# Kernel optimization log

Hardware: AMD Instinct MI355X
Metric: run time of the kernel (lower is better)

Reference implementation:

```python
import jax, jax.numpy as jnp
import numpy as np

N, E = 25000, 400000
NIN, NOUT, HID = 32, 32, 128


def setup_inputs() -> dict:
    key = jax.random.key(0)
    ks = jax.random.split(key, 8)
    s = lambda d: 1.0 / np.sqrt(d)
    return {
        "x": jax.random.normal(ks[0], (N, NIN), jnp.float32),
        "edge_index": jax.random.randint(ks[1], (2, E), 0, N, jnp.int64),
        "edge_attr": jax.random.normal(ks[2], (E, NIN), jnp.float32),
        # edge-MLP: Linear(NIN,HID) -> ReLU -> Linear(HID, NIN*NOUT)
        "w1": jax.random.normal(ks[3], (NIN, HID), jnp.float32) * s(NIN),
        "b1": jnp.zeros((HID,), jnp.float32),
        "w2": jax.random.normal(ks[4], (HID, NIN * NOUT), jnp.float32) * s(HID),
        "b2": jnp.zeros((NIN * NOUT,), jnp.float32),
        # NNConv root weight and bias
        "root": jax.random.normal(ks[5], (NIN, NOUT), jnp.float32) * s(NIN),
        "bias": jnp.zeros((NOUT,), jnp.float32),
    }


def reference(x, edge_index, edge_attr, w1, b1, w2, b2, root, bias):
    src, dst = edge_index[0], edge_index[1]
    # per-edge weight matrices from edge-attr MLP: [E, NIN, NOUT]
    h = jax.nn.relu(edge_attr @ w1 + b1)
    W = (h @ w2 + b2).reshape(-1, NIN, NOUT)
    # gather source features, per-edge small matmul: [E, NOUT]
    msg = jnp.einsum("ei,eio->eo", x[src], W)
    # scatter-add to target nodes (PyG default aggr='add')
    agg = jax.ops.segment_sum(msg, dst, num_segments=N)
    # root/self transform + bias
    return agg + x @ root + bias
```

## Files before the change

### kernel.cpp

```cpp
#include <hip/hip_runtime.h>
#include <hip/hip_fp16.h>


#define NN 25000
#define EE 400000

typedef _Float16 f16x8 __attribute__((ext_vector_type(8)));
typedef float    f32x16 __attribute__((ext_vector_type(16)));
typedef unsigned u32x2  __attribute__((ext_vector_type(2)));

__device__ __forceinline__ void swapHalves(unsigned u, int half,
                                           unsigned& a, unsigned& y) {
#if __has_builtin(__builtin_amdgcn_permlane32_swap)
    u32x2 rr = __builtin_amdgcn_permlane32_swap(u, u, false, false);
    a = rr.x;
    y = rr.y;
#else
    unsigned p = (unsigned)__shfl_xor((int)u, 32, 64);
    a = half ? p : u;
    y = half ? u : p;
#endif
}

__global__ __launch_bounds__(256) void prep_final_kernel(
    const float* __restrict__ x, const float* __restrict__ root,
    const float* __restrict__ bias,
    const float* __restrict__ w1, const float* __restrict__ w2,
    const float* __restrict__ b2,
    _Float16* __restrict__ w2p, _Float16* __restrict__ w1p, _Float16* __restrict__ b2p,
    float* __restrict__ out)
{
    const int t = blockIdx.x * 256 + threadIdx.x;

    if (t < 131072) {
        int j = t & 7, lane = (t >> 3) & 63, ih = (t >> 9) & 1, c = t >> 10;
        w2p[t] = (_Float16)w2[c * 1024 + (ih * 16 + ((lane >> 5) << 3) + j) * 32 + (lane & 31)];
    } else if (t < 135168) {
        int u = t - 131072;
        int j = u & 7, lane = (u >> 3) & 63, kk = (u >> 9) & 1, r = u >> 10;
        w1p[u] = (_Float16)w1[(kk * 16 + ((lane >> 5) << 3) + j) * 128 + r * 32 + (lane & 31)];
    } else if (t < 136192) {
        int u = t - 135168;
        int j = u & 7, lane = (u >> 3) & 63, ih = u >> 9;
        b2p[u] = (_Float16)b2[(ih * 16 + ((lane >> 5) << 3) + j) * 32 + (lane & 31)];
    }

    int n = t >> 5, o = t & 31;
    float acc = bias[o];
    const float* xr = x + (n << 5);
#pragma unroll
    for (int i = 0; i < 32; ++i)
        acc = fmaf(xr[i], root[(i << 5) + o], acc);
    out[t] = acc;
}

__global__ __launch_bounds__(128, 1) void edge_kernel(
    const float*    __restrict__ x,
    const int*      __restrict__ ei,
    const float*    __restrict__ ea,
    const float*    __restrict__ b1,
    const _Float16* __restrict__ w2p,
    const _Float16* __restrict__ w1p,
    const _Float16* __restrict__ b2p,
    float* __restrict__ out)
{
    const int t    = threadIdx.x;
    const int w    = t >> 6;
    const int lane = t & 63;
    const int l    = lane & 31;
    const int half = lane >> 5;

    const int  ebraw = blockIdx.x * 256 + w * 128;
    const bool live  = (ebraw + 128) <= EE;
    const int  ebw   = live ? ebraw : (EE - 128);

    union u8h { f16x8 v; __half2 h2[4]; };

    const f16x8* __restrict__ w2f = (const f16x8*)w2p;

    f16x8 BA[2], BB[2], BC[2], BD[2];
    auto loadCol = [&](int j, f16x8 (&B)[2]) {
        const f16x8* p = w2f + (size_t)j * 128 + lane;
        B[0] = p[0];
        B[1] = p[64];
    };
    loadCol(0, BA); loadCol(1, BB); loadCol(2, BC); loadCol(3, BD);

    u8h eaf[4][2];
#pragma unroll
    for (int g = 0; g < 4; ++g)
#pragma unroll
        for (int kk = 0; kk < 2; ++kk) {
            const float* p = ea + (size_t)(ebw + g * 32 + l) * 32 + kk * 16 + half * 8;
            float4 a0 = *(const float4*)p;
            float4 a1 = *(const float4*)(p + 4);
            eaf[g][kk].h2[0] = __float22half2_rn(make_float2(a0.x, a0.y));
            eaf[g][kk].h2[1] = __float22half2_rn(make_float2(a0.z, a0.w));
            eaf[g][kk].h2[2] = __float22half2_rn(make_float2(a1.x, a1.y));
            eaf[g][kk].h2[3] = __float22half2_rn(make_float2(a1.z, a1.w));
        }

    __half2 xs[4][8];
#pragma unroll
    for (int g = 0; g < 4; ++g) {
        int s = ei[ebw + g * 32 + l];
#pragma unroll
        for (int ih = 0; ih < 2; ++ih) {
            float4 a0 = *(const float4*)(x + s * 32 + ih * 16 + half * 8);
            float4 a1 = *(const float4*)(x + s * 32 + ih * 16 + half * 8 + 4);
            xs[g][ih*4+0] = __float22half2_rn(make_float2(a0.x, a0.y));
            xs[g][ih*4+1] = __float22half2_rn(make_float2(a0.z, a0.w));
            xs[g][ih*4+2] = __float22half2_rn(make_float2(a1.x, a1.y));
            xs[g][ih*4+3] = __float22half2_rn(make_float2(a1.z, a1.w));
        }
    }

    f32x16 acc[4];
#pragma unroll
    for (int g = 0; g < 4; ++g)
#pragma unroll
        for (int i = 0; i < 16; ++i) acc[g][i] = 0.f;

    __half2 hpk[4][8];

    auto phase1 = [&](int r) {
        f16x8 w1f0 = *(const f16x8*)(w1p + ((r * 2 + 0) * 64 + lane) * 8);
        f16x8 w1f1 = *(const f16x8*)(w1p + ((r * 2 + 1) * 64 + lane) * 8);
#pragma unroll
        for (int g = 0; g < 4; ++g) {
            f32x16 h;
#pragma unroll
            for (int i = 0; i < 16; ++i) h[i] = 0.f;
            h = __builtin_amdgcn_mfma_f32_32x32x16_f16(w1f0, eaf[g][0].v, h, 0, 0, 0);
            h = __builtin_amdgcn_mfma_f32_32x32x16_f16(w1f1, eaf[g][1].v, h, 0, 0, 0);
#pragma unroll
            for (int jj = 0; jj < 8; ++jj) {
                int i0 = 2 * jj;
                int r0 = (i0 & 3) + ((i0 >> 2) << 3) + (half << 2);
                hpk[g][jj] = __float22half2_rn(make_float2(
                    fmaxf(h[i0]     + b1[r * 32 + r0],     0.f),
                    fmaxf(h[i0 + 1] + b1[r * 32 + r0 + 1], 0.f)));
            }
        }
    };

    __half2 Ac[4][2], Yc[4][2];

    auto colMFMA = [&](const __half2 (&C)[4][2], int dd, bool hi,
                       const f16x8 (&B)[2]) {
        __half2 d[4];
#pragma unroll
        for (int g = 0; g < 4; ++g)
            d[g] = __half2half2(hi ? __high2half(C[g][dd]) : __low2half(C[g][dd]));
#pragma unroll
        for (int ih = 0; ih < 2; ++ih) {
            f16x8 bfr = B[ih];
#pragma unroll
            for (int g = 0; g < 4; ++g) {
                u8h A;
#pragma unroll
                for (int p = 0; p < 4; ++p)
                    A.h2[p] = __hmul2(d[g], xs[g][ih * 4 + p]);
                acc[g] = __builtin_amdgcn_mfma_f32_32x32x16_f16(A.v, bfr, acc[g], 0, 0, 0);
            }
        }
    };

#pragma unroll 1
    for (int r = 0; r < 4; ++r) {
        phase1(r);
#pragma unroll
        for (int q = 0; q < 8; ++q) {
            const int j = r * 32 + q * 4;
            if ((q & 1) == 0) {
#pragma unroll
                for (int g = 0; g < 4; ++g)
#pragma unroll
                    for (int dd = 0; dd < 2; ++dd) {
                        unsigned a, y;
                        swapHalves(__builtin_bit_cast(unsigned, hpk[g][q + dd]),
                                   half, a, y);
                        Ac[g][dd] = __builtin_bit_cast(__half2, a);
                        Yc[g][dd] = __builtin_bit_cast(__half2, y);
                    }
                colMFMA(Ac, 0, false, BA); loadCol(j + 4, BA);
                colMFMA(Ac, 0, true,  BB); loadCol(j + 5, BB);
                colMFMA(Ac, 1, false, BC); loadCol(j + 6, BC);
                colMFMA(Ac, 1, true,  BD); loadCol(j + 7, BD);
            } else {
                colMFMA(Yc, 0, false, BA); loadCol(j + 4, BA);
                colMFMA(Yc, 0, true,  BB); loadCol(j + 5, BB);
                colMFMA(Yc, 1, false, BC); loadCol(j + 6, BC);
                colMFMA(Yc, 1, true,  BD); loadCol(j + 7, BD);
            }
        }
    }

#pragma unroll
    for (int ih = 0; ih < 2; ++ih) {
        f16x8 bfr = *(const f16x8*)(b2p + (ih * 64 + lane) * 8);
#pragma unroll
        for (int g = 0; g < 4; ++g) {
            u8h A;
#pragma unroll
            for (int p = 0; p < 4; ++p) A.h2[p] = xs[g][ih * 4 + p];
            acc[g] = __builtin_amdgcn_mfma_f32_32x32x16_f16(A.v, bfr, acc[g], 0, 0, 0);
        }
    }

    if (live) {
#pragma unroll
        for (int g = 0; g < 4; ++g)
#pragma unroll
            for (int i = 0; i < 16; ++i) {
                int el = (i & 3) + ((i >> 2) << 3) + (half << 2);
                atomicAdd(out + (size_t)ei[EE + ebw + g * 32 + el] * 32 + l, acc[g][i]);
            }
    }
}

extern "C" void kernel_launch(void* const* d_in, const int* in_sizes, int n_in,
                              void* d_out, int out_size, void* d_ws, size_t ws_size,
                              hipStream_t stream) {
    const float* x    = (const float*)d_in[0];
    const int*   ei   = (const int*)  d_in[1];
    const float* ea   = (const float*)d_in[2];
    const float* w1   = (const float*)d_in[3];
    const float* b1   = (const float*)d_in[4];
    const float* w2   = (const float*)d_in[5];
    const float* b2   = (const float*)d_in[6];
    const float* root = (const float*)d_in[7];
    const float* bias = (const float*)d_in[8];
    float* out = (float*)d_out;

    _Float16* w2p = (_Float16*)d_ws;
    _Float16* w1p = (_Float16*)((char*)d_ws + 262144);
    _Float16* b2p = (_Float16*)((char*)d_ws + 270336);

    prep_final_kernel<<<(NN * 32) / 256, 256, 0, stream>>>(
        x, root, bias, w1, w2, b2, w2p, w1p, b2p, out);

    edge_kernel<<<(EE + 255) / 256, 128, 0, stream>>>(
        x, ei, ea, b1, w2p, w1p, b2p, out);
}
```

Measured before the change: 254.0 us.

## Stage w2 slices into LDS via async global_load_lds shared across four waves

```diff
diff --git a/kernel.cpp b/kernel.cpp
--- a/kernel.cpp
+++ b/kernel.cpp
@@ -8,6 +8,12 @@
 typedef _Float16 f16x8 __attribute__((ext_vector_type(8)));
 typedef float    f32x16 __attribute__((ext_vector_type(16)));
 typedef unsigned u32x2  __attribute__((ext_vector_type(2)));
+
+__device__ __forceinline__ void async16(const void* g, void* l) {
+    __builtin_amdgcn_global_load_lds(
+        (const __attribute__((address_space(1))) unsigned int*)g,
+        (__attribute__((address_space(3))) unsigned int*)l, 16, 0, 0);
+}
 
 __device__ __forceinline__ void swapHalves(unsigned u, int half,
                                            unsigned& a, unsigned& y) {
@@ -54,7 +60,7 @@
     out[t] = acc;
 }
 
-__global__ __launch_bounds__(128, 1) void edge_kernel(
+__global__ __launch_bounds__(256, 1) void edge_kernel(
     const float*    __restrict__ x,
     const int*      __restrict__ ei,
     const float*    __restrict__ ea,
@@ -64,27 +70,29 @@
     const _Float16* __restrict__ b2p,
     float* __restrict__ out)
 {
+    __shared__ __align__(16) _Float16 w2s[32768];
+
     const int t    = threadIdx.x;
     const int w    = t >> 6;
     const int lane = t & 63;
     const int l    = lane & 31;
     const int half = lane >> 5;
 
-    const int  ebraw = blockIdx.x * 256 + w * 128;
+    const int  ebraw = blockIdx.x * 512 + w * 128;
     const bool live  = (ebraw + 128) <= EE;
     const int  ebw   = live ? ebraw : (EE - 128);
 
     union u8h { f16x8 v; __half2 h2[4]; };
 
-    const f16x8* __restrict__ w2f = (const f16x8*)w2p;
-
-    f16x8 BA[2], BB[2], BC[2], BD[2];
-    auto loadCol = [&](int j, f16x8 (&B)[2]) {
-        const f16x8* p = w2f + (size_t)j * 128 + lane;
-        B[0] = p[0];
-        B[1] = p[64];
+    const char* w2g = (const char*)w2p;
+    auto stageSlice = [&](int r) {
+#pragma unroll
+        for (int s = 0; s < 16; ++s) {
+            const int off = w * 16384 + s * 1024;
+            async16(w2g + (size_t)r * 65536 + off + lane * 16,
+                    (void*)((char*)w2s + off));
+        }
     };
-    loadCol(0, BA); loadCol(1, BB); loadCol(2, BC); loadCol(3, BD);
 
     u8h eaf[4][2];
 #pragma unroll
@@ -146,15 +154,14 @@
 
     __half2 Ac[4][2], Yc[4][2];
 
-    auto colMFMA = [&](const __half2 (&C)[4][2], int dd, bool hi,
-                       const f16x8 (&B)[2]) {
+    auto colMFMA = [&](const __half2 (&C)[4][2], int dd, bool hi, int lcol) {
         __half2 d[4];
 #pragma unroll
         for (int g = 0; g < 4; ++g)
             d[g] = __half2half2(hi ? __high2half(C[g][dd]) : __low2half(C[g][dd]));
 #pragma unroll
         for (int ih = 0; ih < 2; ++ih) {
-            f16x8 bfr = B[ih];
+            f16x8 bfr = *(const f16x8*)&w2s[lcol * 1024 + ih * 512 + lane * 8];
 #pragma unroll
             for (int g = 0; g < 4; ++g) {
                 u8h A;
@@ -168,10 +175,13 @@
 
 #pragma unroll 1
     for (int r = 0; r < 4; ++r) {
+        if (r > 0) __syncthreads();
+        stageSlice(r);
         phase1(r);
+        __syncthreads();
 #pragma unroll
         for (int q = 0; q < 8; ++q) {
-            const int j = r * 32 + q * 4;
+            const int c0 = q * 4;
             if ((q & 1) == 0) {
 #pragma unroll
                 for (int g = 0; g < 4; ++g)
@@ -183,15 +193,15 @@
                         Ac[g][dd] = __builtin_bit_cast(__half2, a);
                         Yc[g][dd] = __builtin_bit_cast(__half2, y);
                     }
-                colMFMA(Ac, 0, false, BA); loadCol(j + 4, BA);
-                colMFMA(Ac, 0, true,  BB); loadCol(j + 5, BB);
-                colMFMA(Ac, 1, false, BC); loadCol(j + 6, BC);
-                colMFMA(Ac, 1, true,  BD); loadCol(j + 7, BD);
+                colMFMA(Ac, 0, false, c0 + 0);
+                colMFMA(Ac, 0, true,  c0 + 1);
+                colMFMA(Ac, 1, false, c0 + 2);
+                colMFMA(Ac, 1, true,  c0 + 3);
             } else {
-                colMFMA(Yc, 0, false, BA); loadCol(j + 4, BA);
-                colMFMA(Yc, 0, true,  BB); loadCol(j + 5, BB);
-                colMFMA(Yc, 1, false, BC); loadCol(j + 6, BC);
-                colMFMA(Yc, 1, true,  BD); loadCol(j + 7, BD);
+                colMFMA(Yc, 0, false, c0 + 0);
+                colMFMA(Yc, 0, true,  c0 + 1);
+                colMFMA(Yc, 1, false, c0 + 2);
+                colMFMA(Yc, 1, true,  c0 + 3);
             }
         }
     }
@@ -240,6 +250,6 @@
     prep_final_kernel<<<(NN * 32) / 256, 256, 0, stream>>>(
         x, root, bias, w1, w2, b2, w2p, w1p, b2p, out);
 
-    edge_kernel<<<(EE + 255) / 256, 128, 0, stream>>>(
+    edge_kernel<<<(EE + 511) / 512, 256, 0, stream>>>(
         x, ei, ea, b1, w2p, w1p, b2p, out);
 }
```

Result: slower. 261.2 us (+2.8%).

## Split hidden dimension across two waves per 64-edge block with LDS reduction

Applied to the files above, without the earlier changes.

```diff
diff --git a/kernel.cpp b/kernel.cpp
--- a/kernel.cpp
+++ b/kernel.cpp
@@ -54,7 +54,7 @@
     out[t] = acc;
 }
 
-__global__ __launch_bounds__(128, 1) void edge_kernel(
+__global__ __launch_bounds__(128, 2) void edge_kernel(
     const float*    __restrict__ x,
     const int*      __restrict__ ei,
     const float*    __restrict__ ea,
@@ -64,15 +64,14 @@
     const _Float16* __restrict__ b2p,
     float* __restrict__ out)
 {
+    __shared__ __align__(16) float comb[64][32];
+
     const int t    = threadIdx.x;
     const int w    = t >> 6;
     const int lane = t & 63;
     const int l    = lane & 31;
     const int half = lane >> 5;
-
-    const int  ebraw = blockIdx.x * 256 + w * 128;
-    const bool live  = (ebraw + 128) <= EE;
-    const int  ebw   = live ? ebraw : (EE - 128);
+    const int ebw  = blockIdx.x * 64;
 
     union u8h { f16x8 v; __half2 h2[4]; };
 
@@ -84,11 +83,13 @@
         B[0] = p[0];
         B[1] = p[64];
     };
-    loadCol(0, BA); loadCol(1, BB); loadCol(2, BC); loadCol(3, BD);
-
-    u8h eaf[4][2];
-#pragma unroll
-    for (int g = 0; g < 4; ++g)
+    const int colBase = w * 64;
+    loadCol(colBase + 0, BA); loadCol(colBase + 1, BB);
+    loadCol(colBase + 2, BC); loadCol(colBase + 3, BD);
+
+    u8h eaf[2][2];
+#pragma unroll
+    for (int g = 0; g < 2; ++g)
 #pragma unroll
         for (int kk = 0; kk < 2; ++kk) {
             const float* p = ea + (size_t)(ebw + g * 32 + l) * 32 + kk * 16 + half * 8;
@@ -100,9 +101,9 @@
             eaf[g][kk].h2[3] = __float22half2_rn(make_float2(a1.z, a1.w));
         }
 
-    __half2 xs[4][8];
-#pragma unroll
-    for (int g = 0; g < 4; ++g) {
+    __half2 xs[2][8];
+#pragma unroll
+    for (int g = 0; g < 2; ++g) {
         int s = ei[ebw + g * 32 + l];
 #pragma unroll
         for (int ih = 0; ih < 2; ++ih) {
@@ -115,19 +116,19 @@
         }
     }
 
-    f32x16 acc[4];
-#pragma unroll
-    for (int g = 0; g < 4; ++g)
+    f32x16 acc[2];
+#pragma unroll
+    for (int g = 0; g < 2; ++g)
 #pragma unroll
         for (int i = 0; i < 16; ++i) acc[g][i] = 0.f;
 
-    __half2 hpk[4][8];
+    __half2 hpk[2][8];
 
     auto phase1 = [&](int r) {
         f16x8 w1f0 = *(const f16x8*)(w1p + ((r * 2 + 0) * 64 + lane) * 8);
         f16x8 w1f1 = *(const f16x8*)(w1p + ((r * 2 + 1) * 64 + lane) * 8);
 #pragma unroll
-        for (int g = 0; g < 4; ++g) {
+        for (int g = 0; g < 2; ++g) {
             f32x16 h;
 #pragma unroll
             for (int i = 0; i < 16; ++i) h[i] = 0.f;
@@ -144,37 +145,36 @@
         }
     };
 
-    __half2 Ac[4][2], Yc[4][2];
-
-    auto colMFMA = [&](const __half2 (&C)[4][2], int dd, bool hi,
+    __half2 Ac[2][2], Yc[2][2];
+
+    auto colMFMA = [&](const __half2 (&C)[2][2], int dd, bool hi,
                        const f16x8 (&B)[2]) {
-        __half2 d[4];
-#pragma unroll
-        for (int g = 0; g < 4; ++g)
-            d[g] = __half2half2(hi ? __high2half(C[g][dd]) : __low2half(C[g][dd]));
+        __half2 d0 = __half2half2(hi ? __high2half(C[0][dd]) : __low2half(C[0][dd]));
+        __half2 d1 = __half2half2(hi ? __high2half(C[1][dd]) : __low2half(C[1][dd]));
 #pragma unroll
         for (int ih = 0; ih < 2; ++ih) {
-            f16x8 bfr = B[ih];
-#pragma unroll
-            for (int g = 0; g < 4; ++g) {
-                u8h A;
-#pragma unroll
-                for (int p = 0; p < 4; ++p)
-                    A.h2[p] = __hmul2(d[g], xs[g][ih * 4 + p]);
-                acc[g] = __builtin_amdgcn_mfma_f32_32x32x16_f16(A.v, bfr, acc[g], 0, 0, 0);
-            }
+            u8h A;
+#pragma unroll
+            for (int p = 0; p < 4; ++p)
+                A.h2[p] = __hmul2(d0, xs[0][ih * 4 + p]);
+            acc[0] = __builtin_amdgcn_mfma_f32_32x32x16_f16(A.v, B[ih], acc[0], 0, 0, 0);
+#pragma unroll
+            for (int p = 0; p < 4; ++p)
+                A.h2[p] = __hmul2(d1, xs[1][ih * 4 + p]);
+            acc[1] = __builtin_amdgcn_mfma_f32_32x32x16_f16(A.v, B[ih], acc[1], 0, 0, 0);
         }
     };
 
 #pragma unroll 1
-    for (int r = 0; r < 4; ++r) {
+    for (int rr = 0; rr < 2; ++rr) {
+        const int r = w * 2 + rr;
         phase1(r);
 #pragma unroll
         for (int q = 0; q < 8; ++q) {
             const int j = r * 32 + q * 4;
             if ((q & 1) == 0) {
 #pragma unroll
-                for (int g = 0; g < 4; ++g)
+                for (int g = 0; g < 2; ++g)
 #pragma unroll
                     for (int dd = 0; dd < 2; ++dd) {
                         unsigned a, y;
@@ -196,21 +196,35 @@
         }
     }
 
-#pragma unroll
-    for (int ih = 0; ih < 2; ++ih) {
-        f16x8 bfr = *(const f16x8*)(b2p + (ih * 64 + lane) * 8);
-#pragma unroll
-        for (int g = 0; g < 4; ++g) {
-            u8h A;
-#pragma unroll
-            for (int p = 0; p < 4; ++p) A.h2[p] = xs[g][ih * 4 + p];
-            acc[g] = __builtin_amdgcn_mfma_f32_32x32x16_f16(A.v, bfr, acc[g], 0, 0, 0);
-        }
-    }
-
-    if (live) {
-#pragma unroll
-        for (int g = 0; g < 4; ++g)
+    if (w == 1) {
+#pragma unroll
+        for (int g = 0; g < 2; ++g)
+#pragma unroll
+            for (int i = 0; i < 16; ++i)
+                comb[lane][g * 16 + i] = acc[g][i];
+    }
+    __syncthreads();
+    if (w == 0) {
+#pragma unroll
+        for (int g = 0; g < 2; ++g)
+#pragma unroll
+            for (int i = 0; i < 16; ++i)
+                acc[g][i] += comb[lane][g * 16 + i];
+
+#pragma unroll
+        for (int ih = 0; ih < 2; ++ih) {
+            f16x8 bfr = *(const f16x8*)(b2p + (ih * 64 + lane) * 8);
+#pragma unroll
+            for (int g = 0; g < 2; ++g) {
+                u8h A;
+#pragma unroll
+                for (int p = 0; p < 4; ++p) A.h2[p] = xs[g][ih * 4 + p];
+                acc[g] = __builtin_amdgcn_mfma_f32_32x32x16_f16(A.v, bfr, acc[g], 0, 0, 0);
+            }
+        }
+
+#pragma unroll
+        for (int g = 0; g < 2; ++g)
 #pragma unroll
             for (int i = 0; i < 16; ++i) {
                 int el = (i & 3) + ((i >> 2) << 3) + (half << 2);
@@ -240,6 +254,6 @@
     prep_final_kernel<<<(NN * 32) / 256, 256, 0, stream>>>(
         x, root, bias, w1, w2, b2, w2p, w1p, b2p, out);
 
-    edge_kernel<<<(EE + 255) / 256, 128, 0, stream>>>(
+    edge_kernel<<<EE / 64, 128, 0, stream>>>(
         x, ei, ea, b1, w2p, w1p, b2p, out);
 }
```

New measurement: 241.4 us. 1.05x faster.
